# Kernel optimization log

Measured on AMD Instinct MI355X. Metric: run time of the kernel, lower is better.

Reference implementation:

```python
import jax, jax.numpy as jnp
import numpy as np

B, S, D = 2, 2048, 1024
H = 16
HD = D // H  # 64
SCALE = HD ** 0.5


def setup_inputs() -> dict:
    key = jax.random.key(0)
    ks = jax.random.split(key, 7)
    return {
        "query": jax.random.normal(ks[0], (B, S, D), dtype=jnp.float32),
        "key": jax.random.normal(ks[1], (B, S, D), dtype=jnp.float32),
        "value": jax.random.normal(ks[2], (B, S, D), dtype=jnp.float32),
        "W_qkv_w": jax.random.normal(ks[3], (3 * D, 3 * D), dtype=jnp.float32) * (1.0 / np.sqrt(3 * D)),
        "W_qkv_b": jax.random.normal(ks[4], (3 * D,), dtype=jnp.float32) * 0.02,
        "W_o_w": jax.random.normal(ks[5], (D, D), dtype=jnp.float32) * (1.0 / np.sqrt(D)),
        "W_o_b": jax.random.normal(ks[6], (D,), dtype=jnp.float32) * 0.02,
    }


def _split_heads(x):
    # [B,S,D] -> [B,H,S,HD]
    return x.reshape(B, S, H, HD).transpose(0, 2, 1, 3)


def reference(query, key, value, W_qkv_w, W_qkv_b, W_o_w, W_o_b):
    # fused QKV projection: concat then Linear(3D, 3D)  (torch: x @ W.T + b)
    qkv = jnp.concatenate([query, key, value], axis=-1)
    qkv = qkv @ W_qkv_w.T + W_qkv_b
    q, k, v = jnp.split(qkv, 3, axis=-1)
    q, k, v = _split_heads(q), _split_heads(k), _split_heads(v)
    # naive attention: materializes [B,H,S,S]
    scores = jnp.einsum('bhqd,bhkd->bhqk', q, k) / SCALE
    probs = jax.nn.softmax(scores, axis=-1)
    attn = jnp.einsum('bhqk,bhkd->bhqd', probs, v)
    # combine heads: [B,H,S,HD] -> [B,S,D]
    attn = attn.transpose(0, 2, 1, 3).reshape(B, S, D)
    return attn @ W_o_w.T + W_o_b
```

## Files before the change

### kernel.cpp

```cpp
#include <hip/hip_runtime.h>
#include <cmath>

#define BS   2
#define SEQ  2048
#define DM   1024
#define NH   16
#define HD   64
#define D3   3072
#define MROWS 4096
#define KVBLK 64
#define QBLK  128
#define NTILES (SEQ / KVBLK)
#define NCHUNK 2
#define CTILES (NTILES / NCHUNK)

#define CSC 0.18033688011112042f

typedef _Float16 f16;
typedef __attribute__((ext_vector_type(4))) _Float16 half4;
typedef __attribute__((ext_vector_type(8))) _Float16 half8;
typedef __attribute__((ext_vector_type(4))) float f32x4;
typedef unsigned int u32;
typedef __attribute__((ext_vector_type(2))) u32 u32x2;
typedef __attribute__((ext_vector_type(4))) u32 u32x4;

__device__ __forceinline__ void async_cp16(const void* g, void* s) {
    __builtin_amdgcn_global_load_lds(
        (const __attribute__((address_space(1))) u32*)g,
        (__attribute__((address_space(3))) u32*)s, 16, 0, 0);
}

__global__ __launch_bounds__(256) void conv_concat_kernel(
    const float* __restrict__ q, const float* __restrict__ k,
    const float* __restrict__ v, f16* __restrict__ out)
{
    const int seg = blockIdx.x;
    const int row = blockIdx.y;
    const int c   = threadIdx.x * 4;
    const float* src = (seg == 0 ? q : (seg == 1 ? k : v)) + (size_t)row * DM + c;
    float4 x = *(const float4*)src;
    half4 h = {(f16)x.x, (f16)x.y, (f16)x.z, (f16)x.w};
    *(half4*)&out[(size_t)row * D3 + seg * DM + c] = h;
}

__global__ __launch_bounds__(256) void conv_plain_kernel(
    const float* __restrict__ src, f16* __restrict__ dst, int n4)
{
    int i = blockIdx.x * 256 + threadIdx.x;
    const int stride = gridDim.x * 256;
    for (; i < n4; i += stride) {
        float4 x = *(const float4*)&src[(size_t)i * 4];
        half4 h = {(f16)x.x, (f16)x.y, (f16)x.z, (f16)x.w};
        *(half4*)&dst[(size_t)i * 4] = h;
    }
}

#define SWZ4(r) (((r) >> 1) & 3)

template<int KDIM, int NDIM>
__global__ __launch_bounds__(512, 2) void gemm8p_f16_kernel(
    const f16* __restrict__ A, const f16* __restrict__ W,
    const float* __restrict__ bias, f16* __restrict__ Cout)
{
    __shared__ f16 lds[65536];

    const int tid  = threadIdx.x;
    const int lane = tid & 63;
    const int wave = tid >> 6;
    const int l15  = lane & 15;
    const int lg   = lane >> 4;
    const int wm   = wave >> 2;
    const int wn   = wave & 3;

    const int cpx = gridDim.x >> 3;
    const int lid = (blockIdx.x & 7) * cpx + (blockIdx.x >> 3);
    const int NTC = NDIM / 256;
    const int tM0 = (lid / NTC) * 256;
    const int tN0 = (lid % NTC) * 256;

    const int rr  = wave * 16 + (lane >> 2);
    const int cs  = (lane & 3) ^ SWZ4(rr);
    const f16* gA = A + (size_t)(tM0 + rr) * KDIM + cs * 8;
    const f16* gW = W + (size_t)(tN0 + rr) * KDIM + cs * 8;
    const int sbase = wave * 512;

    f32x4 acc[8][4];
#pragma unroll
    for (int i = 0; i < 8; ++i)
#pragma unroll
        for (int j = 0; j < 4; ++j) acc[i][j] = (f32x4){0.f, 0.f, 0.f, 0.f};

    const int fch = lg ^ SWZ4(l15);
    const int aro = (wm * 128 + l15) * 32 + fch * 8;
    const int bro = 32768 + (wn * 64 + l15) * 32 + fch * 8;

    constexpr int NT = KDIM / 64;

#define STAGE_A(S, KS, KT) do {                                               \
    const f16* s_ = gA + (size_t)(KT) * 64 + (KS) * 32;                       \
    f16* d_ = &lds[(S) * 16384 + (KS) * 8192 + sbase];                        \
    async_cp16(s_, d_);                                                       \
    async_cp16(s_ + (size_t)128 * KDIM, d_ + 4096);                           \
} while (0)

#define STAGE_B(S, KS, KT) do {                                               \
    const f16* s_ = gW + (size_t)(KT) * 64 + (KS) * 32;                       \
    f16* d_ = &lds[32768 + (S) * 16384 + (KS) * 8192 + sbase];                \
    async_cp16(s_, d_);                                                       \
    async_cp16(s_ + (size_t)128 * KDIM, d_ + 4096);                           \
} while (0)

#define PHASE(S, KS, MH, VMEND, STAGE_STMT) do {                              \
    const int pb_ = (S) * 16384 + (KS) * 8192;                                \
    half8 af[4];                                                              \
    _Pragma("unroll")                                                         \
    for (int mi = 0; mi < 4; ++mi)                                            \
        af[mi] = *(half8*)&lds[pb_ + aro + ((MH) * 4 + mi) * 512];            \
    if ((MH) == 0) {                                                          \
        _Pragma("unroll")                                                     \
        for (int ni = 0; ni < 4; ++ni)                                        \
            wf[ni] = *(half8*)&lds[pb_ + bro + ni * 512];                     \
    }                                                                         \
    STAGE_STMT;                                                               \
    __builtin_amdgcn_s_barrier();                                             \
    asm volatile("s_waitcnt lgkmcnt(0)" ::: "memory");                        \
    __builtin_amdgcn_sched_barrier(0);                                        \
    __builtin_amdgcn_s_setprio(1);                                            \
    _Pragma("unroll")                                                         \
    for (int mi = 0; mi < 4; ++mi)                                            \
        _Pragma("unroll")                                                     \
        for (int ni = 0; ni < 4; ++ni)                                        \
            acc[(MH) * 4 + mi][ni] = __builtin_amdgcn_mfma_f32_16x16x32_f16(  \
                af[mi], wf[ni], acc[(MH) * 4 + mi][ni], 0, 0, 0);             \
    __builtin_amdgcn_s_setprio(0);                                            \
    __builtin_amdgcn_sched_barrier(0);                                        \
    if (VMEND) {                                                              \
        asm volatile("s_waitcnt vmcnt(8)" ::: "memory");                      \
        __builtin_amdgcn_sched_barrier(0);                                    \
    }                                                                         \
    __builtin_amdgcn_s_barrier();                                             \
} while (0)

    STAGE_A(0, 0, 0); STAGE_B(0, 0, 0);
    STAGE_A(0, 1, 0); STAGE_B(0, 1, 0);
    STAGE_A(1, 0, 1); STAGE_B(1, 0, 1);
    asm volatile("s_waitcnt vmcnt(8)" ::: "memory");
    __builtin_amdgcn_s_barrier();

    half8 wf[4];
    for (int it = 0; it < NT / 2; ++it) {
        const int t   = 2 * it;
        const int t1c = t + 1;
        const int t2c = (t + 2 < NT) ? t + 2 : NT - 1;
        const int t3c = (t + 3 < NT) ? t + 3 : NT - 1;
        PHASE(0, 0, 0, false, STAGE_A(1, 1, t1c));
        PHASE(0, 0, 1, true,  STAGE_B(1, 1, t1c));
        PHASE(0, 1, 0, false, STAGE_A(0, 0, t2c));
        PHASE(0, 1, 1, true,  STAGE_B(0, 0, t2c));
        PHASE(1, 0, 0, false, STAGE_A(0, 1, t2c));
        PHASE(1, 0, 1, true,  STAGE_B(0, 1, t2c));
        PHASE(1, 1, 0, false, STAGE_A(1, 0, t3c));
        PHASE(1, 1, 1, true,  STAGE_B(1, 0, t3c));
    }

#undef PHASE
#undef STAGE_A
#undef STAGE_B

    float bv[4];
#pragma unroll
    for (int ni = 0; ni < 4; ++ni) bv[ni] = bias[tN0 + wn * 64 + ni * 16 + l15];

#pragma unroll
    for (int mi = 0; mi < 8; ++mi)
#pragma unroll
        for (int ni = 0; ni < 4; ++ni)
#pragma unroll
            for (int r = 0; r < 4; ++r) {
                const int m   = tM0 + wm * 128 + mi * 16 + lg * 4 + r;
                const int col = tN0 + wn * 64 + ni * 16 + l15;
                Cout[(size_t)m * NDIM + col] = (f16)(acc[mi][ni][r] + bv[ni]);
            }
}

__global__ __launch_bounds__(128) void gemm_out_kernel(
    const f16* __restrict__ A, const f16* __restrict__ W,
    const float* __restrict__ bias, float* __restrict__ Cout)
{
    constexpr int KDIM = DM, NDIM = DM;
    __shared__ f16 As[64 * 32];
    __shared__ f16 Ws[128 * 32];

    const int tid  = threadIdx.x;
    const int lane = tid & 63;
    const int wave = tid >> 6;
    const int l15  = lane & 15;
    const int lg   = lane >> 4;

    const int cpx = gridDim.x >> 3;
    const int lid = (blockIdx.x & 7) * cpx + (blockIdx.x >> 3);
    const int NT2 = NDIM / 128;
    const int tM0 = (lid / NT2) * 64;
    const int tN0 = (lid % NT2) * 128;

    const int srow = lane >> 2;
    const int sch  = lane & 3;
    const int ssc  = sch ^ ((srow >> 1) & 3);

    const f16* gA0 = A + (size_t)(tM0 + wave * 32      + srow) * KDIM + ssc * 8;
    const f16* gA1 = A + (size_t)(tM0 + wave * 32 + 16 + srow) * KDIM + ssc * 8;
    const f16* gW0 = W + (size_t)(tN0 + wave * 64      + srow) * KDIM + ssc * 8;
    const f16* gW1 = W + (size_t)(tN0 + wave * 64 + 16 + srow) * KDIM + ssc * 8;
    const f16* gW2 = W + (size_t)(tN0 + wave * 64 + 32 + srow) * KDIM + ssc * 8;
    const f16* gW3 = W + (size_t)(tN0 + wave * 64 + 48 + srow) * KDIM + ssc * 8;
    f16* lA0 = &As[(wave * 32)      * 32];
    f16* lA1 = &As[(wave * 32 + 16) * 32];
    f16* lW0 = &Ws[(wave * 64)      * 32];
    f16* lW1 = &Ws[(wave * 64 + 16) * 32];
    f16* lW2 = &Ws[(wave * 64 + 32) * 32];
    f16* lW3 = &Ws[(wave * 64 + 48) * 32];

    f32x4 acc[4][4];
#pragma unroll
    for (int i = 0; i < 4; ++i)
#pragma unroll
        for (int j = 0; j < 4; ++j) acc[i][j] = (f32x4){0.f, 0.f, 0.f, 0.f};

    const int fsw = (lg ^ ((l15 >> 1) & 3)) * 8;
    int aoff[4], woff[4];
#pragma unroll
    for (int mi = 0; mi < 4; ++mi) aoff[mi] = (mi * 16 + l15) * 32 + fsw;
#pragma unroll
    for (int ni = 0; ni < 4; ++ni) woff[ni] = (wave * 64 + ni * 16 + l15) * 32 + fsw;

    for (int k0 = 0; k0 < KDIM; k0 += 32) {
        __syncthreads();
        async_cp16(gA0 + k0, lA0);
        async_cp16(gA1 + k0, lA1);
        async_cp16(gW0 + k0, lW0);
        async_cp16(gW1 + k0, lW1);
        async_cp16(gW2 + k0, lW2);
        async_cp16(gW3 + k0, lW3);
        __syncthreads();

        half8 af[4], wf[4];
#pragma unroll
        for (int mi = 0; mi < 4; ++mi) af[mi] = *(half8*)&As[aoff[mi]];
#pragma unroll
        for (int ni = 0; ni < 4; ++ni) wf[ni] = *(half8*)&Ws[woff[ni]];
#pragma unroll
        for (int mi = 0; mi < 4; ++mi)
#pragma unroll
            for (int ni = 0; ni < 4; ++ni)
                acc[mi][ni] = __builtin_amdgcn_mfma_f32_16x16x32_f16(
                    af[mi], wf[ni], acc[mi][ni], 0, 0, 0);
    }

    float bv[4];
#pragma unroll
    for (int ni = 0; ni < 4; ++ni) bv[ni] = bias[tN0 + wave * 64 + ni * 16 + l15];

#pragma unroll
    for (int mi = 0; mi < 4; ++mi)
#pragma unroll
        for (int ni = 0; ni < 4; ++ni)
#pragma unroll
            for (int r = 0; r < 4; ++r) {
                const int m   = tM0 + mi * 16 + lg * 4 + r;
                const int col = tN0 + wave * 64 + ni * 16 + l15;
                Cout[(size_t)m * NDIM + col] = acc[mi][ni][r] + bv[ni];
            }
}


#define V_STORE(VtN, va, vb) do {                                             \
    u32x4 aw_ = __builtin_bit_cast(u32x4, va);                                \
    u32x4 bw_ = __builtin_bit_cast(u32x4, vb);                                \
    _Pragma("unroll")                                                         \
    for (int wd_ = 0; wd_ < 4; ++wd_) {                                       \
        u32 lo_ = __builtin_amdgcn_perm(bw_[wd_], aw_[wd_], 0x05040100u);     \
        u32 hi_ = __builtin_amdgcn_perm(bw_[wd_], aw_[wd_], 0x07060302u);     \
        const int dl_ = vd0 + 2 * wd_;                                        \
        const int dh_ = dl_ + 1;                                              \
        *(u32*)&VtN[dl_ * KVBLK + (((vp >> 2) ^ (dl_ & 7) ^ (dl_ >> 3)) * 8)  \
                    + 2 * (vp & 3)] = lo_;                                    \
        *(u32*)&VtN[dh_ * KVBLK + (((vp >> 2) ^ (dh_ & 7) ^ (dh_ >> 3)) * 8)  \
                    + 2 * (vp & 3)] = hi_;                                    \
    }                                                                         \
} while (0)

#define ATTN_STEP(KhC, VtC, KhN, VtN, TT, PF) do {                            \
    half8 va_ = {}, vb_ = {};                                                 \
    if (PF) {                                                                 \
        const size_t nro_ = (size_t)((TT) + 1) * KVBLK;                       \
        async_cp16(kxsrc + (nro_ + wave * 16 +     krow_l) * D3,              \
                   &KhN[(wave * 16) * HD]);                                   \
        async_cp16(kxsrc + (nro_ + wave * 16 + 8 + krow_l) * D3,              \
                   &KhN[(wave * 16 + 8) * HD]);                               \
        va_ = *(const half8*)(vsrc0 + nro_ * D3);                             \
        vb_ = *(const half8*)(vsrc0 + nro_ * D3 + D3);                        \
    }                                                                         \
    f32x4 sc[2][4];                                                           \
    _Pragma("unroll")                                                         \
    for (int rt = 0; rt < 2; ++rt)                                            \
        _Pragma("unroll")                                                     \
        for (int ct = 0; ct < 4; ++ct) sc[rt][ct] = (f32x4){0.f,0.f,0.f,0.f}; \
    __builtin_amdgcn_s_setprio(1);                                            \
    _Pragma("unroll")                                                         \
    for (int ct = 0; ct < 4; ++ct) {                                          \
        const int krow = ct * 16 + l15;                                       \
        _Pragma("unroll")                                                     \
        for (int ks = 0; ks < 2; ++ks) {                                      \
            half8 kf = *(half8*)&KhC[krow * HD +                              \
                                     (((ks * 4 + lg) ^ (krow & 7)) * 8)];     \
            _Pragma("unroll")                                                 \
            for (int rt = 0; rt < 2; ++rt)                                    \
                sc[rt][ct] = __builtin_amdgcn_mfma_f32_16x16x32_f16(          \
                    kf, qf[rt][ks], sc[rt][ct], 0, 0, 0);                     \
        }                                                                     \
    }                                                                         \
    __builtin_amdgcn_s_setprio(0);                                            \
    _Pragma("unroll")                                                         \
    for (int rt = 0; rt < 2; ++rt) {                                          \
        float mt = sc[rt][0][0];                                              \
        _Pragma("unroll")                                                     \
        for (int ct = 0; ct < 4; ++ct)                                        \
            _Pragma("unroll")                                                 \
            for (int r = 0; r < 4; ++r)                                       \
                if (ct || r) mt = fmaxf(mt, sc[rt][ct][r]);                   \
        mt = fmaxf(mt, __shfl_xor(mt, 16));                                   \
        mt = fmaxf(mt, __shfl_xor(mt, 32));                                   \
        const float mn = fmaxf(mrun[rt], mt * CSC);                           \
        const float alpha = exp2f(mrun[rt] - mn);                             \
        mrun[rt] = mn;                                                        \
        float pv_[4][4];                                                      \
        float ls = 0.f;                                                       \
        _Pragma("unroll")                                                     \
        for (int ct = 0; ct < 4; ++ct)                                        \
            _Pragma("unroll")                                                 \
            for (int r = 0; r < 4; ++r) {                                     \
                pv_[ct][r] = exp2f(fmaf(sc[rt][ct][r], CSC, -mn));            \
                ls += pv_[ct][r];                                             \
            }                                                                 \
        ls += __shfl_xor(ls, 16);                                             \
        ls += __shfl_xor(ls, 32);                                             \
        lrun[rt] = lrun[rt] * alpha + ls;                                     \
        _Pragma("unroll")                                                     \
        for (int dct = 0; dct < 4; ++dct)                                     \
            _Pragma("unroll")                                                 \
            for (int r = 0; r < 4; ++r) oacc[rt][dct][r] *= alpha;            \
        const int prow_ = pbase + (rt * 16 + l15) * KVBLK;                    \
        _Pragma("unroll")                                                     \
        for (int ct = 0; ct < 4; ++ct) {                                      \
            u32 w01 = __builtin_bit_cast(u32,                                 \
                __builtin_amdgcn_cvt_pkrtz(pv_[ct][0], pv_[ct][1]));          \
            u32 w23 = __builtin_bit_cast(u32,                                 \
                __builtin_amdgcn_cvt_pkrtz(pv_[ct][2], pv_[ct][3]));          \
            *(u32x2*)&Pl[prow_ + ((4 * ct + lg) ^ l15) * 4] =                 \
                (u32x2){w01, w23};                                            \
        }                                                                     \
    }                                                                         \
    __builtin_amdgcn_s_setprio(1);                                            \
    _Pragma("unroll")                                                         \
    for (int ks2 = 0; ks2 < 2; ++ks2) {                                       \
        half8 pa[2];                                                          \
        _Pragma("unroll")                                                     \
        for (int rt = 0; rt < 2; ++rt) {                                      \
            const int prow_ = pbase + (rt * 16 + l15) * KVBLK;                \
            half4 plA_ = *(half4*)&Pl[prow_ + ((8 * ks2 + 2 * lg)     ^ l15) * 4]; \
            half4 plB_ = *(half4*)&Pl[prow_ + ((8 * ks2 + 2 * lg + 1) ^ l15) * 4]; \
            pa[rt] = __builtin_shufflevector(plA_, plB_, 0,1,2,3,4,5,6,7);    \
        }                                                                     \
        _Pragma("unroll")                                                     \
        for (int dct = 0; dct < 4; ++dct) {                                   \
            const int d = dct * 16 + l15;                                     \
            half8 vf = *(half8*)&VtC[d * KVBLK +                              \
                        (((ks2 * 4 + lg) ^ (d & 7) ^ (d >> 3)) * 8)];         \
            _Pragma("unroll")                                                 \
            for (int rt = 0; rt < 2; ++rt)                                    \
                oacc[rt][dct] = __builtin_amdgcn_mfma_f32_16x16x32_f16(       \
                    vf, pa[rt], oacc[rt][dct], 0, 0, 0);                      \
        }                                                                     \
    }                                                                         \
    __builtin_amdgcn_s_setprio(0);                                            \
    if (PF) { V_STORE(VtN, va_, vb_); }                                       \
    __syncthreads();                                                          \
} while (0)

__global__ __launch_bounds__(256, 2) void attn_mfma_kernel(
    const f16* __restrict__ qkvh, f16* __restrict__ U, float2* __restrict__ ml)
{
    __shared__ f16 Kh0[KVBLK * HD];
    __shared__ f16 Kh1[KVBLK * HD];
    __shared__ f16 Vt0[HD * KVBLK];
    __shared__ f16 Vt1[HD * KVBLK];
    __shared__ f16 Pl[4 * 32 * KVBLK];

    const int tid  = threadIdx.x;
    const int lane = tid & 63;
    const int wave = tid >> 6;
    const int l15  = lane & 15;
    const int lg   = lane >> 4;

    const int nq  = SEQ / QBLK;
    const int cpx = gridDim.x >> 3;
    const int lid = (blockIdx.x & 7) * cpx + (blockIdx.x >> 3);
    const int qc = lid % nq;
    const int hc = lid / nq;
    const int c  = hc & (NCHUNK - 1);
    const int bh = hc / NCHUNK;
    const int h  = bh % NH;
    const int b  = bh / NH;
    const int q0 = qc * QBLK + wave * 32;
    const size_t bS = (size_t)b * SEQ;
    const int t0 = c * CTILES;
    const int tEnd = t0 + CTILES;

    const int krow_l = lane >> 3;
    const int kschk  = (lane & 7) ^ krow_l;
    const f16* kxsrc = qkvh + bS * D3 + DM + h * HD + kschk * 8;

    const int vp  = tid >> 3;
    const int vd0 = (tid & 7) * 8;
    const f16* vsrc0 = qkvh + (bS + 2 * vp) * D3 + 2 * DM + h * HD + vd0;

    half8 qf[2][2];
#pragma unroll
    for (int rt = 0; rt < 2; ++rt)
#pragma unroll
        for (int ks = 0; ks < 2; ++ks)
            qf[rt][ks] = *(const half8*)&qkvh[(bS + q0 + rt * 16 + l15) * D3 +
                                              h * HD + ks * 32 + lg * 8];

    f32x4 oacc[2][4];
#pragma unroll
    for (int rt = 0; rt < 2; ++rt)
#pragma unroll
        for (int dct = 0; dct < 4; ++dct) oacc[rt][dct] = (f32x4){0.f, 0.f, 0.f, 0.f};

    float mrun[2], lrun[2];
#pragma unroll
    for (int rt = 0; rt < 2; ++rt) { mrun[rt] = -INFINITY; lrun[rt] = 0.f; }

    const int pbase = wave * 32 * KVBLK;

    {
        const size_t r0 = (size_t)t0 * KVBLK;
        async_cp16(kxsrc + (r0 + wave * 16 +     krow_l) * D3, &Kh0[(wave * 16) * HD]);
        async_cp16(kxsrc + (r0 + wave * 16 + 8 + krow_l) * D3, &Kh0[(wave * 16 + 8) * HD]);
        half8 va_ = *(const half8*)(vsrc0 + r0 * D3);
        half8 vb_ = *(const half8*)(vsrc0 + r0 * D3 + D3);
        V_STORE(Vt0, va_, vb_);
        __syncthreads();
    }

    for (int t = t0; t < tEnd; t += 2) {
        ATTN_STEP(Kh0, Vt0, Kh1, Vt1, t, true);
        ATTN_STEP(Kh1, Vt1, Kh0, Vt0, t + 1, (t + 2) < tEnd);
    }

    f16* Uc = U + (size_t)c * MROWS * DM;
#pragma unroll
    for (int rt = 0; rt < 2; ++rt) {
        const int qq = q0 + rt * 16 + l15;
#pragma unroll
        for (int dct = 0; dct < 4; ++dct) {
            half4 o;
#pragma unroll
            for (int r = 0; r < 4; ++r) o[r] = (f16)oacc[rt][dct][r];
            *(half4*)&Uc[(bS + qq) * DM + h * HD + dct * 16 + 4 * lg] = o;
        }
        if (lg == 0)
            ml[(((size_t)c * BS + b) * NH + h) * SEQ + qq] =
                make_float2(mrun[rt], lrun[rt]);
    }
}

__global__ __launch_bounds__(128) void attn_combine_kernel(
    const f16* __restrict__ U, const float2* __restrict__ ml,
    f16* __restrict__ outh)
{
    const int row = blockIdx.x;
    const int b = row >> 11;
    const int q = row & (SEQ - 1);
    const int d = threadIdx.x * 8;
    const int h = d >> 6;

    const float2 a1 = ml[(((size_t)0 * BS + b) * NH + h) * SEQ + q];
    const float2 a2 = ml[(((size_t)1 * BS + b) * NH + h) * SEQ + q];
    const float m  = fmaxf(a1.x, a2.x);
    float w1 = exp2f(a1.x - m);
    float w2 = exp2f(a2.x - m);
    const float inv = 1.f / (a1.y * w1 + a2.y * w2);
    w1 *= inv; w2 *= inv;

    half8 u1 = *(const half8*)&U[(size_t)row * DM + d];
    half8 u2 = *(const half8*)&U[(size_t)(MROWS + row) * DM + d];
    half8 o;
#pragma unroll
    for (int e = 0; e < 8; ++e)
        o[e] = (f16)((float)u1[e] * w1 + (float)u2[e] * w2);
    *(half8*)&outh[(size_t)row * DM + d] = o;
}

extern "C" void kernel_launch(void* const* d_in, const int* in_sizes, int n_in,
                              void* d_out, int out_size, void* d_ws, size_t ws_size,
                              hipStream_t stream) {
    const float* q    = (const float*)d_in[0];
    const float* k    = (const float*)d_in[1];
    const float* v    = (const float*)d_in[2];
    const float* Wqkv = (const float*)d_in[3];
    const float* bqkv = (const float*)d_in[4];
    const float* Wo   = (const float*)d_in[5];
    const float* bo   = (const float*)d_in[6];
    float* out = (float*)d_out;

    char* ws = (char*)d_ws;
    f16* Ain    = (f16*)ws;
    f16* U      = (f16*)ws;
    f16* attn_h = (f16*)ws;
    f16* Wo_h   = (f16*)(ws + 16777216);
    float2* ml  = (float2*)(ws + 20971520);
    f16* Wqkv_h = (f16*)(ws + 25165824);
    f16* qkv_h  = (f16*)(ws + 44040192);

    conv_concat_kernel<<<dim3(3, MROWS), 256, 0, stream>>>(q, k, v, Ain);
    conv_plain_kernel<<<2048, 256, 0, stream>>>(Wqkv, Wqkv_h, D3 * D3 / 4);

    gemm8p_f16_kernel<D3, D3><<<dim3((MROWS / 256) * (D3 / 256)), 512, 0, stream>>>(
        Ain, Wqkv_h, bqkv, qkv_h);

    attn_mfma_kernel<<<dim3(BS * NH * (SEQ / QBLK) * NCHUNK), 256, 0, stream>>>(
        qkv_h, U, ml);

    conv_plain_kernel<<<512, 256, 0, stream>>>(Wo, Wo_h, DM * DM / 4);

    attn_combine_kernel<<<dim3(MROWS), 128, 0, stream>>>(U, ml, attn_h);

    gemm_out_kernel<<<dim3((MROWS / 64) * (DM / 128)), 128, 0, stream>>>(
        attn_h, Wo_h, bo, out);
}
```

Baseline: 203.8 us.

## Redistribute softmax probabilities via cross-lane shuffles instead of LDS staging

Replaces the P-tile round trip through shared memory (packed f16 stores to Pl followed by reloads) with register-level cross-lane shuffles that rearrange the S-accumulator layout into the MFMA A-operand layout. This drops the 16KB Pl LDS buffer, and the launch bounds are raised from 2 to 4 blocks per SM to use the freed LDS for occupancy. The trade is twelve ds_bpermute-style shuffles plus selects per row tile, and tighter register limits under 4-block occupancy that may cause spills.

```diff
diff --git a/kernel.cpp b/kernel.cpp
--- a/kernel.cpp
+++ b/kernel.cpp
@@ -320,6 +320,7 @@
         }                                                                     \
     }                                                                         \
     __builtin_amdgcn_s_setprio(0);                                            \
+    half8 pa[2][2];                                                           \
     _Pragma("unroll")                                                         \
     for (int rt = 0; rt < 2; ++rt) {                                          \
         float mt = sc[rt][0][0];                                              \
@@ -349,28 +350,42 @@
         for (int dct = 0; dct < 4; ++dct)                                     \
             _Pragma("unroll")                                                 \
             for (int r = 0; r < 4; ++r) oacc[rt][dct][r] *= alpha;            \
-        const int prow_ = pbase + (rt * 16 + l15) * KVBLK;                    \
+           \
+        u32 pk_[4][2];                                                        \
         _Pragma("unroll")                                                     \
         for (int ct = 0; ct < 4; ++ct) {                                      \
-            u32 w01 = __builtin_bit_cast(u32,                                 \
+            pk_[ct][0] = __builtin_bit_cast(u32,                              \
                 __builtin_amdgcn_cvt_pkrtz(pv_[ct][0], pv_[ct][1]));          \
-            u32 w23 = __builtin_bit_cast(u32,                                 \
+            pk_[ct][1] = __builtin_bit_cast(u32,                              \
                 __builtin_amdgcn_cvt_pkrtz(pv_[ct][2], pv_[ct][3]));          \
-            *(u32x2*)&Pl[prow_ + ((4 * ct + lg) ^ l15) * 4] =                 \
-                (u32x2){w01, w23};                                            \
         }                                                                     \
+        u32 q02_[4] = {pk_[0][0], pk_[0][1], pk_[2][0], pk_[2][1]};           \
+        u32 q13_[4] = {pk_[1][0], pk_[1][1], pk_[3][0], pk_[3][1]};           \
+        u32 own_[4], v32_[4], r16_[4], r32_[4], r48_[4], A_[4], B_[4];        \
+        _Pragma("unroll")                                                     \
+        for (int j = 0; j < 4; ++j) {                                         \
+            own_[j] = hi_lg ? q13_[j] : q02_[j];                              \
+            v32_[j] = hi_lg ? q02_[j] : q13_[j];                              \
+        }                                                                     \
+        _Pragma("unroll")                                                     \
+        for (int j = 0; j < 4; ++j) {                                         \
+            r16_[j] = __shfl_xor((int)own_[j], 16);                           \
+            r32_[j] = __shfl_xor((int)v32_[j], 32);                           \
+            r48_[j] = __shfl_xor((int)v32_[j], 48);                           \
+        }                                                                     \
+        _Pragma("unroll")                                                     \
+        for (int j = 0; j < 4; ++j) {                                         \
+            A_[j] = diag_lg ? (hi_lg ? r32_[j] : r48_[j])                     \
+                            : (hi_lg ? r16_[j] : own_[j]);                    \
+            B_[j] = diag_lg ? (hi_lg ? r48_[j] : r32_[j])                     \
+                            : (hi_lg ? own_[j] : r16_[j]);                    \
+        }                                                                     \
+        pa[rt][0] = __builtin_bit_cast(half8, (u32x4){A_[0], A_[1], B_[0], B_[1]}); \
+        pa[rt][1] = __builtin_bit_cast(half8, (u32x4){A_[2], A_[3], B_[2], B_[3]}); \
     }                                                                         \
     __builtin_amdgcn_s_setprio(1);                                            \
     _Pragma("unroll")                                                         \
     for (int ks2 = 0; ks2 < 2; ++ks2) {                                       \
-        half8 pa[2];                                                          \
-        _Pragma("unroll")                                                     \
-        for (int rt = 0; rt < 2; ++rt) {                                      \
-            const int prow_ = pbase + (rt * 16 + l15) * KVBLK;                \
-            half4 plA_ = *(half4*)&Pl[prow_ + ((8 * ks2 + 2 * lg)     ^ l15) * 4]; \
-            half4 plB_ = *(half4*)&Pl[prow_ + ((8 * ks2 + 2 * lg + 1) ^ l15) * 4]; \
-            pa[rt] = __builtin_shufflevector(plA_, plB_, 0,1,2,3,4,5,6,7);    \
-        }                                                                     \
         _Pragma("unroll")                                                     \
         for (int dct = 0; dct < 4; ++dct) {                                   \
             const int d = dct * 16 + l15;                                     \
@@ -379,7 +394,7 @@
             _Pragma("unroll")                                                 \
             for (int rt = 0; rt < 2; ++rt)                                    \
                 oacc[rt][dct] = __builtin_amdgcn_mfma_f32_16x16x32_f16(       \
-                    vf, pa[rt], oacc[rt][dct], 0, 0, 0);                      \
+                    vf, pa[rt][ks2], oacc[rt][dct], 0, 0, 0);                 \
         }                                                                     \
     }                                                                         \
     __builtin_amdgcn_s_setprio(0);                                            \
@@ -387,20 +402,21 @@
     __syncthreads();                                                          \
 } while (0)
 
-__global__ __launch_bounds__(256, 2) void attn_mfma_kernel(
+__global__ __launch_bounds__(256, 4) void attn_mfma_kernel(
     const f16* __restrict__ qkvh, f16* __restrict__ U, float2* __restrict__ ml)
 {
     __shared__ f16 Kh0[KVBLK * HD];
     __shared__ f16 Kh1[KVBLK * HD];
     __shared__ f16 Vt0[HD * KVBLK];
     __shared__ f16 Vt1[HD * KVBLK];
-    __shared__ f16 Pl[4 * 32 * KVBLK];
 
     const int tid  = threadIdx.x;
     const int lane = tid & 63;
     const int wave = tid >> 6;
     const int l15  = lane & 15;
     const int lg   = lane >> 4;
+    const int hi_lg   = (lg >> 1) & 1;
+    const int diag_lg = (lg ^ (lg >> 1)) & 1;
 
     const int nq  = SEQ / QBLK;
     const int cpx = gridDim.x >> 3;
@@ -442,8 +458,6 @@
 #pragma unroll
     for (int rt = 0; rt < 2; ++rt) { mrun[rt] = -INFINITY; lrun[rt] = 0.f; }
 
-    const int pbase = wave * 32 * KVBLK;
-
     {
         const size_t r0 = (size_t)t0 * KVBLK;
         async_cp16(kxsrc + (r0 + wave * 16 +     krow_l) * D3, &Kh0[(wave * 16) * HD]);
```

New measurement: 253.6 us. 1.24x slower.
